# Performance work log

Measured on AMD Instinct MI355X. Metric: run time of the kernel, lower is better.

The kernel has to match this reference:

```python
import jax, jax.numpy as jnp
import numpy as np

N_GLIMPSES = 3
GS = 64          # glimpse_size
IN_C = 3         # input_channels
B, H, W = 64, 512, 512


def get_glimpses(image, loc):
    """Multi-scale glimpse extraction (tf.image.extract_glimpse, centered+normalized)
    followed by antialiased bicubic resize to GS x GS, concatenated on channels."""
    b, h, w, c = image.shape
    max_size = GS * 2 ** (N_GLIMPSES - 1)
    padded = jnp.pad(image, ((0, 0), (max_size, max_size), (max_size, max_size), (0, 0)))
    hp, wp = h + 2 * max_size, w + 2 * max_size
    # normalized+centered offsets: (-1,-1)=upper-left, (1,1)=lower-right of padded image
    center = (loc + 1.0) * 0.5 * jnp.array([hp, wp], dtype=jnp.float32)  # (y, x) per batch
    glimpses = []
    for i in range(N_GLIMPSES):
        s = GS * 2 ** i  # current crop size (python int, static)
        tl = jnp.round(center - 0.5 * s).astype(jnp.int32)
        tl = jnp.clip(tl, 0, jnp.array([hp - s, wp - s], dtype=jnp.int32))

        def slice_one(img, yx):
            return jax.lax.dynamic_slice(img, (yx[0], yx[1], 0), (s, s, c))

        g = jax.vmap(slice_one)(padded, tl)                      # [B, s, s, C]
        g = jax.image.resize(g, (b, GS, GS, c), method='cubic')  # antialiased bicubic
        glimpses.append(g)
    return jnp.concatenate(glimpses, axis=-1)  # [B, GS, GS, N_GLIMPSES*C]


def setup_inputs() -> dict:
    key = jax.random.key(0)
    ks = jax.random.split(key, 10)
    image = jax.random.uniform(ks[0], (B, H, W, IN_C), dtype=jnp.float32)
    loc = jax.random.uniform(ks[1], (B, 2), dtype=jnp.float32, minval=-1.0, maxval=1.0)
    cg = N_GLIMPSES * IN_C
    # conv1_g: full-kernel (GS x GS) valid conv -> 1x1x128
    Wg = jax.random.normal(ks[2], (GS, GS, cg, 128), dtype=jnp.float32) * (1.0 / np.sqrt(GS * GS * cg))
    bg = jnp.zeros((128,), jnp.float32)
    # conv1_l: 1x1 conv on loc [B,1,1,2]
    Wl = jax.random.normal(ks[3], (2, 128), dtype=jnp.float32) * (1.0 / np.sqrt(2.0))
    bl = jnp.zeros((128,), jnp.float32)
    # out: 1x1 conv 128 -> 256
    Wo = jax.random.normal(ks[4], (128, 256), dtype=jnp.float32) * (1.0 / np.sqrt(128.0))
    bo = jnp.zeros((256,), jnp.float32)
    return {"image": image, "loc": loc, "Wg": Wg, "bg": bg, "Wl": Wl, "bl": bl, "Wo": Wo, "bo": bo}


def reference(image, loc, Wg, bg, Wl, bl, Wo, bo):
    glimpses = get_glimpses(image, loc)  # [B, GS, GS, N_GLIMPSES*IN_C]
    # conv1_g with kernel == glimpse size and VALID padding == dense contraction over hwc
    x1 = jax.nn.relu(jnp.einsum('bhwc,hwck->bk', glimpses, Wg) + bg)  # [B,128]
    x2 = jax.nn.relu(loc @ Wl + bl)                                   # [B,128]
    out = jax.nn.relu((x1 + x2) @ Wo + bo)                            # [B,256]
    return out
```

## Files before the change

kernel.cpp:

```cpp
#include <hip/hip_runtime.h>

#define IMG_H 512
#define IMG_W 512
#define PAD   256
#define HP    1024
#define BATCH 64
#define KTOT  36864
#define KTILE 128
#define KB    16
#define NTILES 288

__device__ __forceinline__ float keys_cubic(float x) {
  if (x >= 2.0f) return 0.0f;
  if (x >= 1.0f) return ((-0.5f * x + 2.5f) * x - 4.0f) * x + 2.0f;
  return ((1.5f * x - 2.5f) * x) * x + 1.0f;
}

template <int KS>
__device__ __forceinline__ void glimpse_resize_body(
    const float* __restrict__ imb, int b, int y, int tly, int tlx,
    float* __restrict__ G, int tid, float* tmp) {
  constexpr int S  = 64 * KS;
  constexpr int NT = 4 * KS;
  const float fks = (float)KS;

  float sy  = ((float)y + 0.5f) * fks - 0.5f;
  int   iy0 = (int)ceilf(sy - 2.0f * fks);
  float wy[NT];
  float wsum = 0.0f;
#pragma unroll
  for (int t = 0; t < NT; ++t) {
    int i = iy0 + t;
    float w = 0.0f;
    if (i >= 0 && i < S) w = keys_cubic(fabsf(sy - (float)i) / fks);
    wy[t] = w;
    wsum += w;
  }
  float winv = 1.0f / wsum;
#pragma unroll
  for (int t = 0; t < NT; ++t) wy[t] *= winv;

  for (int e = tid; e < S * 3; e += 256) {
    int xcol = e / 3;
    int c    = e - 3 * xcol;
    int px   = tlx - PAD + xcol;
    float a = 0.0f;
    if ((unsigned)px < (unsigned)IMG_W) {
      const float* colp = imb + (px * 3 + c);
#pragma unroll
      for (int t = 0; t < NT; ++t) {
        int py = tly + iy0 + t - PAD;
        if ((unsigned)py < (unsigned)IMG_H)
          a = fmaf(wy[t], colp[py * (IMG_W * 3)], a);
      }
    }
    tmp[e] = a;
  }
  __syncthreads();

  if (tid < 192) {
    int xo = tid / 3;
    int c  = tid - 3 * xo;
    float sx  = ((float)xo + 0.5f) * fks - 0.5f;
    int   ix0 = (int)ceilf(sx - 2.0f * fks);
    float a = 0.0f, wsx = 0.0f;
#pragma unroll
    for (int t = 0; t < NT; ++t) {
      int i = ix0 + t;
      if (i >= 0 && i < S) {
        float w = keys_cubic(fabsf(sx - (float)i) / fks);
        wsx += w;
        a = fmaf(w, tmp[i * 3 + c], a);
      }
    }
    constexpr int sc = (KS == 2) ? 1 : 2;
    G[(((size_t)b * 64 + y) * 64 + xo) * 9 + 3 * sc + c] = a / wsx;
  }
}

__global__ __launch_bounds__(256) void glimpse_kernel(
    const float* __restrict__ img, const float* __restrict__ loc,
    float* __restrict__ G) {
  __shared__ float tmp[768];
  int blk = blockIdx.x;
  int y   = blk & 63;
  int t3  = blk >> 6;
  int sc  = t3 % 3;
  int b   = t3 / 3;
  int tid = threadIdx.x;

  float cy = (loc[2 * b] + 1.0f) * 0.5f * 1024.0f;
  float cx = (loc[2 * b + 1] + 1.0f) * 0.5f * 1024.0f;
  int s   = 64 << sc;
  int tly = min(max((int)rintf(cy - 0.5f * (float)s), 0), HP - s);
  int tlx = min(max((int)rintf(cx - 0.5f * (float)s), 0), HP - s);
  const float* imb = img + (size_t)b * (IMG_H * IMG_W * 3);

  if (sc == 0) {
    if (tid < 192) {
      int x = tid / 3, c = tid - 3 * (tid / 3);
      int py = tly + y - PAD, px = tlx + x - PAD;
      float v = 0.0f;
      if ((unsigned)py < (unsigned)IMG_H && (unsigned)px < (unsigned)IMG_W)
        v = imb[(py * IMG_W + px) * 3 + c];
      G[(((size_t)b * 64 + y) * 64 + x) * 9 + c] = v;
    }
  } else if (sc == 1) {
    glimpse_resize_body<2>(imb, b, y, tly, tlx, G, tid, tmp);
  } else {
    glimpse_resize_body<4>(imb, b, y, tly, tlx, G, tid, tmp);
  }
}

__global__ __launch_bounds__(256) void gemm_kernel(
    const float* __restrict__ G, const float* __restrict__ Wg,
    float* __restrict__ partials) {
  const int tile = blockIdx.x;
  const int tid  = threadIdx.x;
  const int tn   = tid & 15;
  const int tm   = tid >> 4;
  __shared__ float Gs[KB][64];
  __shared__ float Ws[KB][128];

  const int gb = tid >> 2;
  const int gj = (tid & 3) * 4;
  const int wr = tid >> 4;
  const int wc = (tid & 15) * 8;
  const size_t gbase = (size_t)gb * KTOT + (size_t)tile * KTILE + gj;
  const size_t wbase = ((size_t)tile * KTILE + wr) * 128 + wc;

  float4 g4 = *(const float4*)(G + gbase);
  float4 wa = *(const float4*)(Wg + wbase);
  float4 wb = *(const float4*)(Wg + wbase + 4);

  float acc[4][8];
#pragma unroll
  for (int mi = 0; mi < 4; ++mi)
#pragma unroll
    for (int ni = 0; ni < 8; ++ni) acc[mi][ni] = 0.0f;

  constexpr int NCHUNK = KTILE / KB;
#pragma unroll
  for (int chunk = 0; chunk < NCHUNK; ++chunk) {
    Gs[gj + 0][gb] = g4.x;
    Gs[gj + 1][gb] = g4.y;
    Gs[gj + 2][gb] = g4.z;
    Gs[gj + 3][gb] = g4.w;
    *(float4*)&Ws[wr][wc]     = wa;
    *(float4*)&Ws[wr][wc + 4] = wb;
    __syncthreads();
    if (chunk + 1 < NCHUNK) {
      g4 = *(const float4*)(G + gbase + (chunk + 1) * KB);
      wa = *(const float4*)(Wg + wbase + (size_t)(chunk + 1) * KB * 128);
      wb = *(const float4*)(Wg + wbase + (size_t)(chunk + 1) * KB * 128 + 4);
    }
#pragma unroll
    for (int j = 0; j < KB; ++j) {
      float4 gv = *(const float4*)&Gs[j][tm * 4];
      float4 w0 = *(const float4*)&Ws[j][tn * 8];
      float4 w1 = *(const float4*)&Ws[j][tn * 8 + 4];
      float gm[4] = {gv.x, gv.y, gv.z, gv.w};
      float wn[8] = {w0.x, w0.y, w0.z, w0.w, w1.x, w1.y, w1.z, w1.w};
#pragma unroll
      for (int mi = 0; mi < 4; ++mi)
#pragma unroll
        for (int ni = 0; ni < 8; ++ni)
          acc[mi][ni] = fmaf(gm[mi], wn[ni], acc[mi][ni]);
    }
    __syncthreads();
  }

#pragma unroll
  for (int mi = 0; mi < 4; ++mi) {
    int m = tm * 4 + mi;
    float4 v0 = make_float4(acc[mi][0], acc[mi][1], acc[mi][2], acc[mi][3]);
    float4 v1 = make_float4(acc[mi][4], acc[mi][5], acc[mi][6], acc[mi][7]);
    float* dst = partials + ((size_t)tile * 64 + m) * 128 + tn * 8;
    *(float4*)dst       = v0;
    *(float4*)(dst + 4) = v1;
  }
}

__global__ __launch_bounds__(256) void finalize_kernel(
    const float* __restrict__ partials, const float* __restrict__ loc,
    const float* __restrict__ bg, const float* __restrict__ Wl,
    const float* __restrict__ bl, const float* __restrict__ Wo,
    const float* __restrict__ bo, float* __restrict__ out) {
  int b   = blockIdx.x;
  int tid = threadIdx.x;
  int k    = tid & 127;
  int half = tid >> 7;

  float s = 0.0f;
  for (int t = half; t < NTILES; t += 2)
    s += partials[((size_t)t * 64 + b) * 128 + k];

  __shared__ float red[256];
  __shared__ float h[128];
  red[tid] = s;
  __syncthreads();
  if (tid < 128) {
    float ss = red[tid] + red[tid + 128];
    float x1 = fmaxf(ss + bg[tid], 0.0f);
    float x2 = fmaxf(fmaf(loc[2 * b], Wl[tid],
                          fmaf(loc[2 * b + 1], Wl[128 + tid], bl[tid])),
                     0.0f);
    h[tid] = x1 + x2;
  }
  __syncthreads();
  {
    int n = tid;
    float a = bo[n];
#pragma unroll 8
    for (int kk = 0; kk < 128; ++kk) a = fmaf(h[kk], Wo[kk * 256 + n], a);
    out[(size_t)b * 256 + n] = fmaxf(a, 0.0f);
  }
}

extern "C" void kernel_launch(void* const* d_in, const int* in_sizes, int n_in,
                              void* d_out, int out_size, void* d_ws, size_t ws_size,
                              hipStream_t stream) {
  const float* img = (const float*)d_in[0];
  const float* loc = (const float*)d_in[1];
  const float* Wg  = (const float*)d_in[2];
  const float* bg  = (const float*)d_in[3];
  const float* Wl  = (const float*)d_in[4];
  const float* bl  = (const float*)d_in[5];
  const float* Wo  = (const float*)d_in[6];
  const float* bo  = (const float*)d_in[7];
  float* out = (float*)d_out;

  float* ws = (float*)d_ws;
  float* G        = ws;
  float* partials = ws + 2359296;

  glimpse_kernel<<<BATCH * 3 * 64, 256, 0, stream>>>(img, loc, G);
  gemm_kernel<<<NTILES, 256, 0, stream>>>(G, Wg, partials);
  finalize_kernel<<<BATCH, 256, 0, stream>>>(partials, loc, bg, Wl, bl, Wo, bo, out);
}
```

Measured before the change: 349.7 us.

## Double-buffer GEMM shared tiles, retile K to 256 blocks, make partials batch-major

The GEMM kernel now alternates between two shared-memory buffers, which removes the trailing barrier in each K chunk. K is split into 256 tiles of 144 instead of 288 tiles of 128, so every block fits in one wave across the CUs. Partials are stored batch-major so the finalize reduction reads one contiguous region per batch row. The trade-offs are doubled shared memory, longer per-block work, and a reliance on one barrier per chunk being enough to prevent write-after-read hazards.

```diff
diff --git a/kernel.cpp b/kernel.cpp
--- a/kernel.cpp
+++ b/kernel.cpp
@@ -6,9 +6,9 @@
 #define HP    1024
 #define BATCH 64
 #define KTOT  36864
-#define KTILE 128
+#define KTILE 144
 #define KB    16
-#define NTILES 288
+#define NTILES 256
 
 __device__ __forceinline__ float keys_cubic(float x) {
   if (x >= 2.0f) return 0.0f;
@@ -119,8 +119,8 @@
   const int tid  = threadIdx.x;
   const int tn   = tid & 15;
   const int tm   = tid >> 4;
-  __shared__ float Gs[KB][64];
-  __shared__ float Ws[KB][128];
+  __shared__ float Gs[2][KB][64];
+  __shared__ float Ws[2][KB][128];
 
   const int gb = tid >> 2;
   const int gj = (tid & 3) * 4;
@@ -142,12 +142,13 @@
   constexpr int NCHUNK = KTILE / KB;
 #pragma unroll
   for (int chunk = 0; chunk < NCHUNK; ++chunk) {
-    Gs[gj + 0][gb] = g4.x;
-    Gs[gj + 1][gb] = g4.y;
-    Gs[gj + 2][gb] = g4.z;
-    Gs[gj + 3][gb] = g4.w;
-    *(float4*)&Ws[wr][wc]     = wa;
-    *(float4*)&Ws[wr][wc + 4] = wb;
+    const int buf = chunk & 1;
+    Gs[buf][gj + 0][gb] = g4.x;
+    Gs[buf][gj + 1][gb] = g4.y;
+    Gs[buf][gj + 2][gb] = g4.z;
+    Gs[buf][gj + 3][gb] = g4.w;
+    *(float4*)&Ws[buf][wr][wc]     = wa;
+    *(float4*)&Ws[buf][wr][wc + 4] = wb;
     __syncthreads();
     if (chunk + 1 < NCHUNK) {
       g4 = *(const float4*)(G + gbase + (chunk + 1) * KB);
@@ -156,9 +157,9 @@
     }
 #pragma unroll
     for (int j = 0; j < KB; ++j) {
-      float4 gv = *(const float4*)&Gs[j][tm * 4];
-      float4 w0 = *(const float4*)&Ws[j][tn * 8];
-      float4 w1 = *(const float4*)&Ws[j][tn * 8 + 4];
+      float4 gv = *(const float4*)&Gs[buf][j][tm * 4];
+      float4 w0 = *(const float4*)&Ws[buf][j][tn * 8];
+      float4 w1 = *(const float4*)&Ws[buf][j][tn * 8 + 4];
       float gm[4] = {gv.x, gv.y, gv.z, gv.w};
       float wn[8] = {w0.x, w0.y, w0.z, w0.w, w1.x, w1.y, w1.z, w1.w};
 #pragma unroll
@@ -167,17 +168,14 @@
         for (int ni = 0; ni < 8; ++ni)
           acc[mi][ni] = fmaf(gm[mi], wn[ni], acc[mi][ni]);
     }
-    __syncthreads();
   }
 
 #pragma unroll
   for (int mi = 0; mi < 4; ++mi) {
     int m = tm * 4 + mi;
-    float4 v0 = make_float4(acc[mi][0], acc[mi][1], acc[mi][2], acc[mi][3]);
-    float4 v1 = make_float4(acc[mi][4], acc[mi][5], acc[mi][6], acc[mi][7]);
-    float* dst = partials + ((size_t)tile * 64 + m) * 128 + tn * 8;
-    *(float4*)dst       = v0;
-    *(float4*)(dst + 4) = v1;
+    float* dst = partials + ((size_t)m * NTILES + tile) * 128 + tn * 8;
+    *(float4*)dst       = make_float4(acc[mi][0], acc[mi][1], acc[mi][2], acc[mi][3]);
+    *(float4*)(dst + 4) = make_float4(acc[mi][4], acc[mi][5], acc[mi][6], acc[mi][7]);
   }
 }
 
@@ -191,9 +189,10 @@
   int k    = tid & 127;
   int half = tid >> 7;
 
+  const float* base = partials + (size_t)b * NTILES * 128;
   float s = 0.0f;
   for (int t = half; t < NTILES; t += 2)
-    s += partials[((size_t)t * 64 + b) * 128 + k];
+    s += base[t * 128 + k];
 
   __shared__ float red[256];
   __shared__ float h[128];
```

New measurement: 344.1 us. About the same (-1.6%).
